# Optimization experiments

Measured on AMD Instinct MI355X. Metric: run time of the kernel, lower is better.

Reference implementation:

```python
import jax, jax.numpy as jnp
import numpy as np
import math

DIM = 2048
N_HEADS = 16
HEAD_DIM = DIM // N_HEADS
B, S = 2, 2048
EPS = 1e-6


def rms_norm(x, w):
    return x * jax.lax.rsqrt(jnp.mean(x * x, axis=-1, keepdims=True) + EPS) * w


def rotate(x, cos, sin):
    x1, x2 = jnp.split(x, 2, axis=-1)
    rotated = jnp.concatenate((-x2, x1), axis=-1)
    return x * cos + rotated * sin


def setup_inputs() -> dict:
    key = jax.random.key(0)
    ks = jax.random.split(key, 16)
    half = HEAD_DIM // 2
    inv_freq = 1.0 / (10000.0 ** (jnp.arange(0, half, dtype=jnp.float32) / half))
    t = jnp.arange(S, dtype=jnp.float32)
    freqs = jnp.einsum('s,d->sd', t, inv_freq)
    emb = jnp.concatenate((freqs, freqs), axis=-1)  # [S, HEAD_DIM]
    cos = jnp.cos(emb)[None, None]  # [1,1,S,HEAD_DIM]
    sin = jnp.sin(emb)[None, None]
    # causal additive mask [1,1,S,S]
    causal = jnp.triu(jnp.full((S, S), -1e9, dtype=jnp.float32), k=1)[None, None]
    sc = 0.02
    return {
        'x': jax.random.normal(ks[0], (B, S, DIM), jnp.float32),
        'cos': cos,
        'sin': sin,
        'mask': causal,
        'attn_norm_w': jnp.ones((DIM,), jnp.float32),
        'ffn_norm_w': jnp.ones((DIM,), jnp.float32),
        'wq': jax.random.normal(ks[1], (DIM, DIM), jnp.float32) * sc,
        'wk': jax.random.normal(ks[2], (DIM, DIM), jnp.float32) * sc,
        'wv': jax.random.normal(ks[3], (DIM, DIM), jnp.float32) * sc,
        'wo': jax.random.normal(ks[4], (DIM, DIM), jnp.float32) * sc,
        'w1': jax.random.normal(ks[5], (DIM, 4 * DIM), jnp.float32) * sc,
        'w2': jax.random.normal(ks[6], (4 * DIM, DIM), jnp.float32) * sc,
        'w3': jax.random.normal(ks[7], (DIM, 4 * DIM), jnp.float32) * sc,
    }


def reference(x, cos, sin, mask, attn_norm_w, ffn_norm_w, wq, wk, wv, wo, w1, w2, w3):
    b, s, d = x.shape
    h = rms_norm(x, attn_norm_w)
    q = (h @ wq).reshape(b, s, N_HEADS, HEAD_DIM).transpose(0, 2, 1, 3)
    k = (h @ wk).reshape(b, s, N_HEADS, HEAD_DIM).transpose(0, 2, 1, 3)
    v = (h @ wv).reshape(b, s, N_HEADS, HEAD_DIM).transpose(0, 2, 1, 3)
    q = rotate(q, cos, sin)
    k = rotate(k, cos, sin)
    attn = jnp.einsum('bhqd,bhkd->bhqk', q, k) / math.sqrt(HEAD_DIM)
    attn = attn + mask
    attn = jax.nn.softmax(attn, axis=-1)
    out = jnp.einsum('bhqk,bhkd->bhqd', attn, v)
    out = out.transpose(0, 2, 1, 3).reshape(b, s, d)
    x = x + out @ wo
    h = rms_norm(x, ffn_norm_w)
    x = x + (jax.nn.silu(h @ w1) * (h @ w3)) @ w2
    return x
```

## Files before the change

### kernel.cpp

```cpp
#include <hip/hip_runtime.h>

#define DIM 2048
#define HDIM 128
#define NH 16
#define SEQ 2048
#define BATCH 2
#define MROWS (BATCH*SEQ)
#define QKP 6144

typedef __attribute__((ext_vector_type(8))) short short8;
typedef __attribute__((ext_vector_type(4))) float f32x4;

template<int N> struct ic { static constexpr int value = N; };

__device__ __forceinline__ unsigned short f2bf(float f) {
  union { float f; unsigned u; } v; v.f = f;
  unsigned r = v.u + 0x7FFFu + ((v.u >> 16) & 1u);
  return (unsigned short)(r >> 16);
}
__device__ __forceinline__ float bf2f(unsigned short b) {
  union { unsigned u; float f; } v; v.u = ((unsigned)b) << 16;
  return v.f;
}

__device__ __forceinline__ void gload16(const void* g, void* l) {
  __builtin_amdgcn_global_load_lds((const __attribute__((address_space(1))) unsigned int*)g,
                                   (__attribute__((address_space(3))) unsigned int*)l,
                                   16, 0, 0);
}

__global__ __launch_bounds__(256) void rmsnorm_kernel(const float* __restrict__ x,
                                                      const float* __restrict__ w,
                                                      unsigned short* __restrict__ out) {
  const int row = blockIdx.x;
  const int t = threadIdx.x;
  const float* xr = x + (size_t)row * DIM;
  float4 v0 = ((const float4*)xr)[t*2];
  float4 v1 = ((const float4*)xr)[t*2+1];
  float ss = v0.x*v0.x + v0.y*v0.y + v0.z*v0.z + v0.w*v0.w
           + v1.x*v1.x + v1.y*v1.y + v1.z*v1.z + v1.w*v1.w;
  #pragma unroll
  for (int i = 1; i < 64; i <<= 1) ss += __shfl_xor(ss, i);
  __shared__ float red[4];
  if ((t & 63) == 0) red[t >> 6] = ss;
  __syncthreads();
  float sum = red[0] + red[1] + red[2] + red[3];
  float sc = rsqrtf(sum * (1.0f/DIM) + 1e-6f);
  const float* wr = w + t*8;
  unsigned short ob[8];
  ob[0] = f2bf(v0.x*sc*wr[0]); ob[1] = f2bf(v0.y*sc*wr[1]);
  ob[2] = f2bf(v0.z*sc*wr[2]); ob[3] = f2bf(v0.w*sc*wr[3]);
  ob[4] = f2bf(v1.x*sc*wr[4]); ob[5] = f2bf(v1.y*sc*wr[5]);
  ob[6] = f2bf(v1.z*sc*wr[6]); ob[7] = f2bf(v1.w*sc*wr[7]);
  uint4 pk;
  pk.x = (unsigned)ob[0] | ((unsigned)ob[1] << 16);
  pk.y = (unsigned)ob[2] | ((unsigned)ob[3] << 16);
  pk.z = (unsigned)ob[4] | ((unsigned)ob[5] << 16);
  pk.w = (unsigned)ob[6] | ((unsigned)ob[7] << 16);
  *((uint4*)(out + (size_t)row*DIM + t*8)) = pk;
}

__global__ __launch_bounds__(256) void transpose3_kernel(const float* __restrict__ W0,
                                                         const float* __restrict__ W1,
                                                         const float* __restrict__ W2,
                                                         unsigned short* __restrict__ D0,
                                                         unsigned short* __restrict__ D1,
                                                         unsigned short* __restrict__ D2,
                                                         int K, int N) {
  const float* W = blockIdx.z == 0 ? W0 : (blockIdx.z == 1 ? W1 : W2);
  unsigned short* D = blockIdx.z == 0 ? D0 : (blockIdx.z == 1 ? D1 : D2);
  __shared__ float tile[64][65];
  const int k0 = blockIdx.x*64, n0 = blockIdx.y*64;
  const int t = threadIdx.x;
  const int rr = t >> 4, cc = (t & 15) * 4;
  #pragma unroll
  for (int i=0;i<4;i++) {
    float4 v = *(const float4*)&W[(size_t)(k0 + rr + i*16)*N + n0 + cc];
    tile[rr+i*16][cc] = v.x; tile[rr+i*16][cc+1] = v.y;
    tile[rr+i*16][cc+2] = v.z; tile[rr+i*16][cc+3] = v.w;
  }
  __syncthreads();
  #pragma unroll
  for (int j=0;j<4;j++) {
    const int n = rr + j*16;
    uint2 pk;
    pk.x = (unsigned)f2bf(tile[cc  ][n]) | ((unsigned)f2bf(tile[cc+1][n]) << 16);
    pk.y = (unsigned)f2bf(tile[cc+2][n]) | ((unsigned)f2bf(tile[cc+3][n]) << 16);
    *(uint2*)&D[(size_t)(n0 + n)*K + k0 + cc] = pk;
  }
}

__global__ __launch_bounds__(256) void transpose_v_kernel(const unsigned short* __restrict__ v,
                                                          int vpitch,
                                                          unsigned short* __restrict__ vt) {
  __shared__ unsigned short tile[32][33];
  const int b = blockIdx.z;
  const int s0 = blockIdx.x*32, c0 = blockIdx.y*32;
  const int tx = threadIdx.x & 31, ty = threadIdx.x >> 5;
  #pragma unroll
  for (int i=0;i<4;i++) tile[ty+i*8][tx] = v[((size_t)(b*SEQ + s0+ty+i*8))*vpitch + c0+tx];
  __syncthreads();
  #pragma unroll
  for (int i=0;i<4;i++) vt[((size_t)(b*DIM + c0+ty+i*8))*SEQ + s0+tx] = tile[tx][ty+i*8];
}

__global__ __launch_bounds__(256) void rope_qk(unsigned short* __restrict__ qk,
                                               const float* __restrict__ cosb,
                                               const float* __restrict__ sinb) {
  const size_t idx = (size_t)blockIdx.x * 256 + threadIdx.x;
  const int d = (int)(idx & 63);
  const int h = (int)((idx >> 6) & 31);
  const int row = (int)(idx >> 11);
  const int s = row & (SEQ-1);
  const size_t base = (size_t)row * QKP + h*HDIM + d;
  float a  = bf2f(qk[base]);
  float bq = bf2f(qk[base+64]);
  float c1 = cosb[s*HDIM + d],    s1 = sinb[s*HDIM + d];
  float c2 = cosb[s*HDIM + d+64], s2 = sinb[s*HDIM + d+64];
  qk[base]    = f2bf(a*c1 - bq*s1);
  qk[base+64] = f2bf(bq*c2 + a*s2);
}

template<int BM, int EPI>
__global__ __launch_bounds__(512, 2) void gemm_pipe(const unsigned short* __restrict__ A,
                                                    const unsigned short* __restrict__ Bt,
                                                    const float* __restrict__ aux,
                                                    void* __restrict__ outp,
                                                    int M, int N, int K) {
  constexpr int HRA = BM/2;
  constexpr int MF  = BM/32;
  constexpr int APP = MF/4;
  constexpr int LA  = BM/128;
  constexpr int AHS = HRA*64;
  constexpr int BB  = 4*AHS;
  extern __shared__ unsigned short ldsd[];
  const int tid = threadIdx.x, l = tid & 63, wid = tid >> 6;
  const int wm = wid >> 2, wn = wid & 3;
  const int lr = l & 15, lg = l >> 4;
  const int bh = wn >> 1, brow0 = (wn & 1)*64;

  const int nbx = N >> 8;
  const int SW = (nbx >= 8) ? (nbx >> 3) : 1;
  const int xcd = (int)blockIdx.x & 7;
  const int ii  = (int)blockIdx.x >> 3;
  const int by = ii / SW;
  const int bx = xcd * SW + (ii % SW);
  const int m0 = by * BM, n0 = bx * 256;

  const int m7 = lr & 7;
  const int jks0 = ((lg    ) ^ m7) << 3;
  const int jks1 = ((4 + lg) ^ m7) << 3;
  const unsigned short* ldsA0 = ldsd + wm*AHS + lr*64;
  const unsigned short* ldsA1 = ldsA0 + 2*AHS;
  const unsigned short* ldsB0 = ldsd + BB + bh*8192 + (brow0+lr)*64;
  const unsigned short* ldsB1 = ldsB0 + 2*8192;

  const int r0 = tid >> 3;
  const int jsw = ((tid & 7) ^ (r0 & 7)) << 3;
  const unsigned short* srcA[2][LA];
  #pragma unroll
  for (int h=0;h<2;h++)
    #pragma unroll
    for (int c=0;c<LA;c++)
      srcA[h][c] = A + (size_t)(m0 + h*HRA + c*64 + r0)*K + jsw;
  const unsigned short* srcB[2][2];
  #pragma unroll
  for (int h=0;h<2;h++)
    #pragma unroll
    for (int c=0;c<2;c++)
      srcB[h][c] = Bt + (size_t)(n0 + h*128 + c*64 + r0)*K + jsw;
  unsigned short* dstL = ldsd + tid*8;

  int kO = 0;
  auto stA = [&](int db, int half, int tiled) {
    #pragma unroll
    for (int c=0;c<LA;c++)
      gload16(srcA[half][c] + kO + tiled, dstL + (db*2+half)*AHS + c*4096);
  };
  auto stB = [&](int db, int half, int tiled) {
    #pragma unroll
    for (int c=0;c<2;c++)
      gload16(srcB[half][c] + kO + tiled, dstL + BB + (db*2+half)*8192 + c*4096);
  };

  f32x4 acc[MF][4] = {};
  short8 bfrag[4][2];
  const int ntile = K >> 6;

  stB(0,0,0); stB(0,1,0);
  stA(0,0,0); stA(0,1,0);
  stB(1,0,64); stB(1,1,64);
  asm volatile("s_waitcnt vmcnt(4)" ::: "memory");
  __builtin_amdgcn_sched_barrier(0);
  __builtin_amdgcn_s_barrier();

  auto phase = [&](auto PC, auto LC) {
    constexpr int P = decltype(PC)::value;
    constexpr int LAST = decltype(LC)::value;
    constexpr int hi = P >> 2;
    constexpr int p  = P & 3;
    if constexpr (p == 0) {
      const unsigned short* bB = hi ? ldsB1 : ldsB0;
      #pragma unroll
      for (int nf=0;nf<4;nf++) {
        bfrag[nf][0] = *(const short8*)(bB + nf*1024 + jks0);
        bfrag[nf][1] = *(const short8*)(bB + nf*1024 + jks1);
      }
    }
    const unsigned short* aB = hi ? ldsA1 : ldsA0;
    short8 afr[APP][2];
    #pragma unroll
    for (int mi=0;mi<APP;mi++) {
      afr[mi][0] = *(const short8*)(aB + (p*APP+mi)*1024 + jks0);
      afr[mi][1] = *(const short8*)(aB + (p*APP+mi)*1024 + jks1);
    }
    if constexpr (P == 0)      stA(1, 0, 64);
    else if constexpr (P == 1) stA(1, 1, 64);
    else if constexpr (!LAST) {
      if constexpr (P == 2)      stB(0, 0, 128);
      else if constexpr (P == 3) stB(0, 1, 128);
      else if constexpr (P == 4) stA(0, 0, 128);
      else if constexpr (P == 5) stA(0, 1, 128);
      else if constexpr (P == 6) stB(1, 0, 192);
      else if constexpr (P == 7) stB(1, 1, 192);
    }
    if constexpr (p == 0) {
      asm volatile("s_waitcnt lgkmcnt(8)" ::: "memory");
    }
    if constexpr (P == 3) {
      if constexpr (LAST) { asm volatile("s_waitcnt vmcnt(0)" ::: "memory"); }
      else                { asm volatile("s_waitcnt vmcnt(4)" ::: "memory"); }
    }
    if constexpr (P == 7 && !LAST) {
      asm volatile("s_waitcnt vmcnt(4)" ::: "memory");
    }
    __builtin_amdgcn_s_barrier();
    asm volatile("s_waitcnt lgkmcnt(0)" ::: "memory");
    __builtin_amdgcn_sched_barrier(0);
    __builtin_amdgcn_s_setprio(1);
    #pragma unroll
    for (int mi=0;mi<APP;mi++)
      #pragma unroll
      for (int nf=0;nf<4;nf++)
        #pragma unroll
        for (int ks=0;ks<2;ks++)
          acc[p*APP+mi][nf] = __builtin_amdgcn_mfma_f32_16x16x32_bf16(afr[mi][ks], bfrag[nf][ks], acc[p*APP+mi][nf], 0,0,0);
    __builtin_amdgcn_s_setprio(0);
    __builtin_amdgcn_s_barrier();
  };

  for (int T = 0; T + 2 < ntile; T += 2, kO += 128) {
    phase(ic<0>{}, ic<0>{}); phase(ic<1>{}, ic<0>{});
    phase(ic<2>{}, ic<0>{}); phase(ic<3>{}, ic<0>{});
    phase(ic<4>{}, ic<0>{}); phase(ic<5>{}, ic<0>{});
    phase(ic<6>{}, ic<0>{}); phase(ic<7>{}, ic<0>{});
  }
  phase(ic<0>{}, ic<1>{}); phase(ic<1>{}, ic<1>{});
  phase(ic<2>{}, ic<1>{}); phase(ic<3>{}, ic<1>{});
  phase(ic<4>{}, ic<1>{}); phase(ic<5>{}, ic<1>{});
  phase(ic<6>{}, ic<1>{}); phase(ic<7>{}, ic<1>{});

  #pragma unroll
  for (int mf = 0; mf < MF; mf++)
    #pragma unroll
    for (int nf = 0; nf < 4; nf++)
      #pragma unroll
      for (int r = 0; r < 4; r++) {
        const int row = m0 + wm*HRA + mf*16 + lg*4 + r;
        const int col = n0 + wn*64 + nf*16 + lr;
        const size_t idx = (size_t)row * N + col;
        if constexpr (EPI == 0) {
          ((unsigned short*)outp)[idx] = f2bf(acc[mf][nf][r]);
        } else if constexpr (EPI == 1) {
          ((float*)outp)[idx] = acc[mf][nf][r] + aux[idx];
        } else {
          float g = acc[mf][nf][r];
          float u = bf2f(((unsigned short*)outp)[idx]);
          float sg = u / (1.0f + __expf(-u));
          ((unsigned short*)outp)[idx] = f2bf(sg * g);
        }
      }
}

template<int EPI>
__global__ __launch_bounds__(256, 3) void gemm_m97(const unsigned short* __restrict__ A,
                                                   const unsigned short* __restrict__ Bt,
                                                   const float* __restrict__ aux,
                                                   void* __restrict__ outp,
                                                   int M, int N, int K) {
  __shared__ unsigned short As[128*32];
  __shared__ unsigned short Bs[128*32];
  const int tid = threadIdx.x, l = tid & 63, w = tid >> 6;
  const int wr = w >> 1, wc = w & 1;
  const int lr = l & 15, lg = l >> 4;

  const int nbx = N >> 7;
  const int SW = ((nbx & 7) == 0) ? (nbx >> 3) : 1;
  const int xcd = (int)blockIdx.x & 7;
  const int ii  = (int)blockIdx.x >> 3;
  const int by = ii / SW;
  const int bx = xcd * SW + (ii % SW);
  const int m0 = by * 128, n0 = bx * 128;

  const int srow = tid >> 2;
  const int jsw = ((tid & 3) ^ (srow & 3)) << 3;
  const unsigned short* srcA[2];
  const unsigned short* srcB[2];
  #pragma unroll
  for (int c=0;c<2;c++) {
    srcA[c] = A  + (size_t)(m0 + c*64 + srow)*K + jsw;
    srcB[c] = Bt + (size_t)(n0 + c*64 + srow)*K + jsw;
  }
  unsigned short* dstA = As + tid*8;
  unsigned short* dstB = Bs + tid*8;

  const int jc = ((lg ^ (lr & 3)) << 3);
  const unsigned short* ldsA = As + (wr*64 + lr)*32 + jc;
  const unsigned short* ldsB = Bs + (wc*64 + lr)*32 + jc;

  f32x4 acc[4][4] = {};
  const int ntile = K >> 5;
  int kO = 0;

  for (int t = 0; t < ntile; ++t, kO += 32) {
    #pragma unroll
    for (int c=0;c<2;c++) {
      gload16(srcA[c] + kO, dstA + c*2048);
      gload16(srcB[c] + kO, dstB + c*2048);
    }
    __syncthreads();
    short8 af[4], bf[4];
    #pragma unroll
    for (int mf=0;mf<4;mf++) af[mf] = *(const short8*)(ldsA + mf*512);
    #pragma unroll
    for (int nf=0;nf<4;nf++) bf[nf] = *(const short8*)(ldsB + nf*512);
    #pragma unroll
    for (int mf=0;mf<4;mf++)
      #pragma unroll
      for (int nf=0;nf<4;nf++)
        acc[mf][nf] = __builtin_amdgcn_mfma_f32_16x16x32_bf16(af[mf], bf[nf], acc[mf][nf], 0,0,0);
    __syncthreads();
  }

  #pragma unroll
  for (int mf = 0; mf < 4; mf++)
    #pragma unroll
    for (int nf = 0; nf < 4; nf++)
      #pragma unroll
      for (int r = 0; r < 4; r++) {
        const int row = m0 + wr*64 + mf*16 + lg*4 + r;
        const int col = n0 + wc*64 + nf*16 + lr;
        const size_t idx = (size_t)row * N + col;
        if constexpr (EPI == 0) {
          ((unsigned short*)outp)[idx] = f2bf(acc[mf][nf][r]);
        } else if constexpr (EPI == 1) {
          ((float*)outp)[idx] = acc[mf][nf][r] + aux[idx];
        } else {
          float g = acc[mf][nf][r];
          float u = bf2f(((unsigned short*)outp)[idx]);
          float sg = u / (1.0f + __expf(-u));
          ((unsigned short*)outp)[idx] = f2bf(sg * g);
        }
      }
}

__global__ __launch_bounds__(256, 2) void attn_kernel(const unsigned short* __restrict__ q,
                                                      const unsigned short* __restrict__ k,
                                                      const unsigned short* __restrict__ vt,
                                                      unsigned short* __restrict__ ao) {
  const int t = threadIdx.x, lane = t & 63, w = t >> 6;
  const int qt = (int)gridDim.x - 1 - (int)blockIdx.x;
  const int bh = blockIdx.y;
  const int b = bh >> 4, h = bh & 15;
  const int lr = lane & 15, lg = lane >> 4;
  const int q0w = qt*128 + w*32;

  __shared__ __attribute__((aligned(16))) unsigned short Kb[64*128];
  __shared__ __attribute__((aligned(16))) unsigned short Vb[128*64];
  __shared__ __attribute__((aligned(16))) unsigned short Ones[16*72];
  __shared__ __attribute__((aligned(16))) unsigned short P[4][32*72];
  unsigned short* pw = &P[w][0];

  for (int idx = t; idx < 16*72; idx += 256) Ones[idx] = (idx < 72) ? 0x3F80 : 0;

  short8 aq[2][4];
  {
    const unsigned short* qp = q + ((size_t)(b*SEQ + q0w + lr))*QKP + h*HDIM;
    #pragma unroll
    for (int mf=0;mf<2;mf++)
      #pragma unroll
      for (int c=0;c<4;c++) aq[mf][c] = *(const short8*)(qp + (size_t)mf*16*QKP + c*32 + lg*8);
  }

  f32x4 accO[2][8] = {};
  f32x4 accO9[2] = {};
  float mrow[2][4];
  #pragma unroll
  for (int mf=0;mf<2;mf++)
    #pragma unroll
    for (int r=0;r<4;r++) mrow[mf][r] = -3.0e38f;

  const float scale = 0.08838834764831845f;
  const unsigned short* kg = k + (size_t)(b*SEQ)*QKP + h*HDIM;
  const unsigned short* vg = vt + (size_t)(bh*HDIM)*SEQ;

  const unsigned short* kga[4]; const unsigned short* vga[4];
  unsigned short* kld[4]; unsigned short* vld[4];
  #pragma unroll
  for (int i=0;i<4;i++) {
    const int D = i*256 + t;
    const int rk = D >> 4, jk = D & 15;
    kga[i] = kg + (size_t)rk*QKP + ((jk ^ (rk & 7)) * 8);
    const int rv = D >> 3, jv = D & 7;
    vga[i] = vg + (size_t)rv*SEQ + ((jv ^ (rv & 7)) * 8);
    kld[i] = &Kb[i*2048 + w*512];
    vld[i] = &Vb[i*2048 + w*512];
  }

  const int KV_END = qt*128 + 128;

  for (int kv0 = 0; kv0 < KV_END; kv0 += 64) {
    #pragma unroll
    for (int i=0;i<4;i++) gload16(kga[i] + (size_t)kv0*QKP, kld[i]);
    #pragma unroll
    for (int i=0;i<4;i++) gload16(vga[i] + kv0, vld[i]);
    __syncthreads();

    if (kv0 < q0w + 32) {
      f32x4 sc[2][4] = {};
      #pragma unroll
      for (int blk=0;blk<4;blk++) {
        const int krow = blk*16 + lr;
        const int sw = (krow & 7) << 3;
        #pragma unroll
        for (int c=0;c<4;c++) {
          short8 bk = *(const short8*)&Kb[krow*128 + ((c*32 + lg*8) ^ sw)];
          sc[0][blk] = __builtin_amdgcn_mfma_f32_16x16x32_bf16(aq[0][c], bk, sc[0][blk], 0,0,0);
          sc[1][blk] = __builtin_amdgcn_mfma_f32_16x16x32_bf16(aq[1][c], bk, sc[1][blk], 0,0,0);
        }
      }
      #pragma unroll
      for (int mf=0;mf<2;mf++)
        #pragma unroll
        for (int blk=0;blk<4;blk++)
          #pragma unroll
          for (int r=0;r<4;r++) sc[mf][blk][r] *= scale;
      if (kv0 + 63 > q0w) {
        #pragma unroll
        for (int mf=0;mf<2;mf++)
          #pragma unroll
          for (int blk=0;blk<4;blk++)
            #pragma unroll
            for (int r=0;r<4;r++)
              if (kv0 + blk*16 + lr > q0w + mf*16 + lg*4 + r) sc[mf][blk][r] = -1.0e30f;
      }
      float pm[2][4];
      #pragma unroll
      for (int mf=0;mf<2;mf++)
        #pragma unroll
        for (int r=0;r<4;r++) {
          float m0 = fmaxf(fmaxf(sc[mf][0][r], sc[mf][1][r]), fmaxf(sc[mf][2][r], sc[mf][3][r]));
          #pragma unroll
          for (int x=1;x<16;x<<=1) m0 = fmaxf(m0, __shfl_xor(m0, x));
          pm[mf][r] = m0;
        }
      int need = 0;
      #pragma unroll
      for (int mf=0;mf<2;mf++)
        #pragma unroll
        for (int r=0;r<4;r++) need |= (pm[mf][r] > mrow[mf][r] + 8.0f) ? 1 : 0;
      if (__any(need)) {
        #pragma unroll
        for (int mf=0;mf<2;mf++)
          #pragma unroll
          for (int r=0;r<4;r++) {
            const float mn = fmaxf(mrow[mf][r], pm[mf][r]);
            const float fc = __expf(mrow[mf][r] - mn);
            mrow[mf][r] = mn;
            #pragma unroll
            for (int n=0;n<8;n++) accO[mf][n][r] *= fc;
            accO9[mf][r] *= fc;
          }
      }
      #pragma unroll
      for (int mf=0;mf<2;mf++)
        #pragma unroll
        for (int blk=0;blk<4;blk++)
          #pragma unroll
          for (int r=0;r<4;r++) {
            const float p = __expf(sc[mf][blk][r] - mrow[mf][r]);
            pw[(mf*16 + lg*4 + r)*72 + blk*16 + lr] = f2bf(p);
          }
      short8 ap[2][2];
      #pragma unroll
      for (int mf=0;mf<2;mf++)
        #pragma unroll
        for (int ks=0;ks<2;ks++) ap[mf][ks] = *(const short8*)&pw[(mf*16 + lr)*72 + ks*32 + lg*8];
      #pragma unroll
      for (int n=0;n<8;n++) {
        #pragma unroll
        for (int ks=0;ks<2;ks++) {
          const int vrow = n*16 + lr;
          const int sw = (vrow & 7) << 3;
          short8 bv = *(const short8*)&Vb[vrow*64 + ((ks*32 + lg*8) ^ sw)];
          accO[0][n] = __builtin_amdgcn_mfma_f32_16x16x32_bf16(ap[0][ks], bv, accO[0][n], 0,0,0);
          accO[1][n] = __builtin_amdgcn_mfma_f32_16x16x32_bf16(ap[1][ks], bv, accO[1][n], 0,0,0);
        }
      }
      #pragma unroll
      for (int ks=0;ks<2;ks++) {
        short8 bv9 = *(const short8*)&Ones[lr*72 + ks*32 + lg*8];
        accO9[0] = __builtin_amdgcn_mfma_f32_16x16x32_bf16(ap[0][ks], bv9, accO9[0], 0,0,0);
        accO9[1] = __builtin_amdgcn_mfma_f32_16x16x32_bf16(ap[1][ks], bv9, accO9[1], 0,0,0);
      }
    }
    __syncthreads();
  }

  #pragma unroll
  for (int mf=0;mf<2;mf++)
    #pragma unroll
    for (int r=0;r<4;r++) {
      const float lv = __shfl(accO9[mf][r], lane & 48);
      const float inv = 1.0f / lv;
      const size_t row = (size_t)(b*SEQ + q0w + mf*16 + lg*4 + r);
      #pragma unroll
      for (int n=0;n<8;n++)
        ao[row*DIM + h*HDIM + n*16 + lr] = f2bf(accO[mf][n][r] * inv);
    }
}

extern "C" void kernel_launch(void* const* d_in, const int* in_sizes, int n_in,
                              void* d_out, int out_size, void* d_ws, size_t ws_size,
                              hipStream_t stream) {
  (void)in_sizes; (void)n_in; (void)out_size; (void)ws_size;
  const float* x    = (const float*)d_in[0];
  const float* cosb = (const float*)d_in[1];
  const float* sinb = (const float*)d_in[2];
  const float* anw  = (const float*)d_in[4];
  const float* fnw  = (const float*)d_in[5];
  const float* wq   = (const float*)d_in[6];
  const float* wk   = (const float*)d_in[7];
  const float* wv   = (const float*)d_in[8];
  const float* wo   = (const float*)d_in[9];
  const float* w1   = (const float*)d_in[10];
  const float* w2   = (const float*)d_in[11];
  const float* w3   = (const float*)d_in[12];

  char* ws = (char*)d_ws;
  const size_t MB = 1048576;
  unsigned short* h     = (unsigned short*)(ws);
  unsigned short* qkvb  = (unsigned short*)(ws + 16*MB);
  unsigned short* mid   = qkvb;
  unsigned short* aob   = (unsigned short*)(ws + 67*MB);
  char* wt              = ws + 84*MB;
  unsigned short* wqkvT = (unsigned short*)wt;
  unsigned short* vtb   = (unsigned short*)wt;
  unsigned short* woT   = (unsigned short*)wt;
  unsigned short* w1T   = (unsigned short*)wt;
  unsigned short* w3T   = (unsigned short*)(wt + 32*MB);
  unsigned short* w2T   = (unsigned short*)wt;
  float* x1f = (float*)d_out;

  dim3 b256(256);
  constexpr unsigned LDS256 = 131072;

  rmsnorm_kernel<<<dim3(MROWS), b256, 0, stream>>>(x, anw, h);

  transpose3_kernel<<<dim3(32,32,3), b256, 0, stream>>>(wq, wk, wv,
      wqkvT, wqkvT + 4194304, wqkvT + 8388608, 2048, 2048);

  gemm_pipe<256,0><<<dim3(384), dim3(512), LDS256, stream>>>(h, wqkvT, nullptr, qkvb, MROWS, 6144, 2048);

  rope_qk<<<dim3(32768), b256, 0, stream>>>(qkvb, cosb, sinb);

  transpose_v_kernel<<<dim3(64,64,2), b256, 0, stream>>>(qkvb + 4096, QKP, vtb);

  attn_kernel<<<dim3(16,32), b256, 0, stream>>>(qkvb, qkvb + 2048, vtb, aob);

  transpose3_kernel<<<dim3(32,32,1), b256, 0, stream>>>(wo, nullptr, nullptr,
      woT, nullptr, nullptr, 2048, 2048);
  gemm_m97<1><<<dim3(512), b256, 0, stream>>>(aob, woT, x, x1f, MROWS, 2048, 2048);

  rmsnorm_kernel<<<dim3(MROWS), b256, 0, stream>>>(x1f, fnw, h);

  transpose3_kernel<<<dim3(32,128,2), b256, 0, stream>>>(w1, w3, nullptr,
      w1T, w3T, nullptr, 2048, 8192);
  gemm_pipe<256,0><<<dim3(512), dim3(512), LDS256, stream>>>(h, w1T, nullptr, mid, MROWS, 8192, 2048);
  gemm_pipe<256,3><<<dim3(512), dim3(512), LDS256, stream>>>(h, w3T, nullptr, mid, MROWS, 8192, 2048);

  transpose3_kernel<<<dim3(128,32,1), b256, 0, stream>>>(w2, nullptr, nullptr,
      w2T, nullptr, nullptr, 8192, 2048);
  gemm_m97<1><<<dim3(512), b256, 0, stream>>>(mid, w2T, x1f, (float*)d_out, MROWS, 2048, 8192);
}
```

Baseline: 880.7 us.

## Add BK=32 pipelined GEMM with 64KB LDS and use gemm_pipe for output projections

Adds a new 256x256-tile GEMM kernel that uses K-tiles of 32 with double-buffered LDS (64KB) and an eight-phase schedule. The schedule interleaves global-to-LDS loads with MFMA bursts, and the kernel now serves the QKV and FFN up-projections. The Wo and W2 projections, which used the simple 128x128 gemm_m97, now go through the existing pipelined gemm_pipe<128> with 512 threads and 256 blocks. The aim is less LDS per block for better occupancy and latency hiding, at the cost of more barriers per K step and fewer blocks on the N=2048 GEMMs.

```diff
diff --git a/kernel.cpp b/kernel.cpp
--- a/kernel.cpp
+++ b/kernel.cpp
@@ -121,6 +121,137 @@
   qk[base+64] = f2bf(bq*c2 + a*s2);
 }
 
+template<int EPI>
+__global__ __launch_bounds__(512, 2) void gemm_pipe32(const unsigned short* __restrict__ A,
+                                                      const unsigned short* __restrict__ Bt,
+                                                      const float* __restrict__ aux,
+                                                      void* __restrict__ outp,
+                                                      int M, int N, int K) {
+  extern __shared__ unsigned short ldsd[];
+  const int tid = threadIdx.x, l = tid & 63, wid = tid >> 6;
+  const int wm = wid >> 2, wn = wid & 3;
+  const int lr = l & 15, lg = l >> 4;
+  const int bh = wn >> 1, brow0 = (wn & 1)*64;
+
+  const int nbx = N >> 8;
+  const int SW = (nbx >= 8) ? (nbx >> 3) : 1;
+  const int xcd = (int)blockIdx.x & 7;
+  const int ii  = (int)blockIdx.x >> 3;
+  const int by = ii / SW;
+  const int bx = xcd * SW + (ii % SW);
+  const int m0 = by * 256, n0 = bx * 256;
+
+  const int jks = ((lg ^ ((lr ^ (lr >> 2)) & 3)) << 3);
+  const unsigned short* ldsA0 = ldsd + wm*4096 + lr*32 + jks;
+  const unsigned short* ldsB0 = ldsd + 16384 + bh*4096 + brow0*32 + lr*32 + jks;
+
+  const int srow = tid >> 2;
+  const int jsw = (((tid & 3) ^ ((srow ^ (srow >> 2)) & 3)) << 3);
+  const unsigned short* srcA[2];
+  const unsigned short* srcB[2];
+  #pragma unroll
+  for (int h=0;h<2;h++) {
+    srcA[h] = A  + (size_t)(m0 + h*128 + srow)*K + jsw;
+    srcB[h] = Bt + (size_t)(n0 + h*128 + srow)*K + jsw;
+  }
+  unsigned short* dstL = ldsd + tid*8;
+
+  int kO = 0;
+  auto stA = [&](int db, int half, int tiled) {
+    gload16(srcA[half] + kO + tiled, dstL + (db*2+half)*4096);
+  };
+  auto stB = [&](int db, int half, int tiled) {
+    gload16(srcB[half] + kO + tiled, dstL + 16384 + (db*2+half)*4096);
+  };
+
+  f32x4 acc[8][4] = {};
+  short8 bfrag[4];
+  const int ntile = K >> 5;
+
+  stB(0,0,0); stB(0,1,0);
+  stA(0,0,0); stA(0,1,0);
+  stB(1,0,32); stB(1,1,32);
+  asm volatile("s_waitcnt vmcnt(2)" ::: "memory");
+  __builtin_amdgcn_sched_barrier(0);
+  __builtin_amdgcn_s_barrier();
+
+  auto phase = [&](auto PC, auto LC) {
+    constexpr int P = decltype(PC)::value;
+    constexpr int LAST = decltype(LC)::value;
+    constexpr int hi = P >> 2;
+    constexpr int p  = P & 3;
+    if constexpr (p == 0) {
+      const unsigned short* bB = ldsB0 + hi*2*4096;
+      #pragma unroll
+      for (int nf=0;nf<4;nf++) bfrag[nf] = *(const short8*)(bB + nf*512);
+    }
+    const unsigned short* aB = ldsA0 + hi*2*4096;
+    short8 afr[2];
+    afr[0] = *(const short8*)(aB + (p*2  )*512);
+    afr[1] = *(const short8*)(aB + (p*2+1)*512);
+    if constexpr (P == 0)      stA(1, 0, 32);
+    else if constexpr (P == 1) stA(1, 1, 32);
+    else if constexpr (!LAST) {
+      if constexpr (P == 2)      stB(0, 0, 64);
+      else if constexpr (P == 3) stB(0, 1, 64);
+      else if constexpr (P == 4) stA(0, 0, 64);
+      else if constexpr (P == 5) stA(0, 1, 64);
+      else if constexpr (P == 6) stB(1, 0, 96);
+      else if constexpr (P == 7) stB(1, 1, 96);
+    }
+    if constexpr (P == 3) {
+      if constexpr (LAST) { asm volatile("s_waitcnt vmcnt(0)" ::: "memory"); }
+      else                { asm volatile("s_waitcnt vmcnt(2)" ::: "memory"); }
+    }
+    if constexpr (P == 7 && !LAST) {
+      asm volatile("s_waitcnt vmcnt(2)" ::: "memory");
+    }
+    __builtin_amdgcn_s_barrier();
+    asm volatile("s_waitcnt lgkmcnt(0)" ::: "memory");
+    __builtin_amdgcn_sched_barrier(0);
+    __builtin_amdgcn_s_setprio(1);
+    #pragma unroll
+    for (int mi=0;mi<2;mi++)
+      #pragma unroll
+      for (int nf=0;nf<4;nf++)
+        acc[p*2+mi][nf] = __builtin_amdgcn_mfma_f32_16x16x32_bf16(afr[mi], bfrag[nf], acc[p*2+mi][nf], 0,0,0);
+    __builtin_amdgcn_s_setprio(0);
+    __builtin_amdgcn_s_barrier();
+  };
+
+  for (int T = 0; T + 2 < ntile; T += 2, kO += 64) {
+    phase(ic<0>{}, ic<0>{}); phase(ic<1>{}, ic<0>{});
+    phase(ic<2>{}, ic<0>{}); phase(ic<3>{}, ic<0>{});
+    phase(ic<4>{}, ic<0>{}); phase(ic<5>{}, ic<0>{});
+    phase(ic<6>{}, ic<0>{}); phase(ic<7>{}, ic<0>{});
+  }
+  phase(ic<0>{}, ic<1>{}); phase(ic<1>{}, ic<1>{});
+  phase(ic<2>{}, ic<1>{}); phase(ic<3>{}, ic<1>{});
+  phase(ic<4>{}, ic<1>{}); phase(ic<5>{}, ic<1>{});
+  phase(ic<6>{}, ic<1>{}); phase(ic<7>{}, ic<1>{});
+
+  #pragma unroll
+  for (int mf = 0; mf < 8; mf++)
+    #pragma unroll
+    for (int nf = 0; nf < 4; nf++)
+      #pragma unroll
+      for (int r = 0; r < 4; r++) {
+        const int row = m0 + wm*128 + mf*16 + lg*4 + r;
+        const int col = n0 + wn*64 + nf*16 + lr;
+        const size_t idx = (size_t)row * N + col;
+        if constexpr (EPI == 0) {
+          ((unsigned short*)outp)[idx] = f2bf(acc[mf][nf][r]);
+        } else if constexpr (EPI == 1) {
+          ((float*)outp)[idx] = acc[mf][nf][r] + aux[idx];
+        } else {
+          float g = acc[mf][nf][r];
+          float u = bf2f(((unsigned short*)outp)[idx]);
+          float sg = u / (1.0f + __expf(-u));
+          ((unsigned short*)outp)[idx] = f2bf(sg * g);
+        }
+      }
+}
+
 template<int BM, int EPI>
 __global__ __launch_bounds__(512, 2) void gemm_pipe(const unsigned short* __restrict__ A,
                                                     const unsigned short* __restrict__ Bt,
@@ -282,88 +413,6 @@
       }
 }
 
-template<int EPI>
-__global__ __launch_bounds__(256, 3) void gemm_m97(const unsigned short* __restrict__ A,
-                                                   const unsigned short* __restrict__ Bt,
-                                                   const float* __restrict__ aux,
-                                                   void* __restrict__ outp,
-                                                   int M, int N, int K) {
-  __shared__ unsigned short As[128*32];
-  __shared__ unsigned short Bs[128*32];
-  const int tid = threadIdx.x, l = tid & 63, w = tid >> 6;
-  const int wr = w >> 1, wc = w & 1;
-  const int lr = l & 15, lg = l >> 4;
-
-  const int nbx = N >> 7;
-  const int SW = ((nbx & 7) == 0) ? (nbx >> 3) : 1;
-  const int xcd = (int)blockIdx.x & 7;
-  const int ii  = (int)blockIdx.x >> 3;
-  const int by = ii / SW;
-  const int bx = xcd * SW + (ii % SW);
-  const int m0 = by * 128, n0 = bx * 128;
-
-  const int srow = tid >> 2;
-  const int jsw = ((tid & 3) ^ (srow & 3)) << 3;
-  const unsigned short* srcA[2];
-  const unsigned short* srcB[2];
-  #pragma unroll
-  for (int c=0;c<2;c++) {
-    srcA[c] = A  + (size_t)(m0 + c*64 + srow)*K + jsw;
-    srcB[c] = Bt + (size_t)(n0 + c*64 + srow)*K + jsw;
-  }
-  unsigned short* dstA = As + tid*8;
-  unsigned short* dstB = Bs + tid*8;
-
-  const int jc = ((lg ^ (lr & 3)) << 3);
-  const unsigned short* ldsA = As + (wr*64 + lr)*32 + jc;
-  const unsigned short* ldsB = Bs + (wc*64 + lr)*32 + jc;
-
-  f32x4 acc[4][4] = {};
-  const int ntile = K >> 5;
-  int kO = 0;
-
-  for (int t = 0; t < ntile; ++t, kO += 32) {
-    #pragma unroll
-    for (int c=0;c<2;c++) {
-      gload16(srcA[c] + kO, dstA + c*2048);
-      gload16(srcB[c] + kO, dstB + c*2048);
-    }
-    __syncthreads();
-    short8 af[4], bf[4];
-    #pragma unroll
-    for (int mf=0;mf<4;mf++) af[mf] = *(const short8*)(ldsA + mf*512);
-    #pragma unroll
-    for (int nf=0;nf<4;nf++) bf[nf] = *(const short8*)(ldsB + nf*512);
-    #pragma unroll
-    for (int mf=0;mf<4;mf++)
-      #pragma unroll
-      for (int nf=0;nf<4;nf++)
-        acc[mf][nf] = __builtin_amdgcn_mfma_f32_16x16x32_bf16(af[mf], bf[nf], acc[mf][nf], 0,0,0);
-    __syncthreads();
-  }
-
-  #pragma unroll
-  for (int mf = 0; mf < 4; mf++)
-    #pragma unroll
-    for (int nf = 0; nf < 4; nf++)
-      #pragma unroll
-      for (int r = 0; r < 4; r++) {
-        const int row = m0 + wr*64 + mf*16 + lg*4 + r;
-        const int col = n0 + wc*64 + nf*16 + lr;
-        const size_t idx = (size_t)row * N + col;
-        if constexpr (EPI == 0) {
-          ((unsigned short*)outp)[idx] = f2bf(acc[mf][nf][r]);
-        } else if constexpr (EPI == 1) {
-          ((float*)outp)[idx] = acc[mf][nf][r] + aux[idx];
-        } else {
-          float g = acc[mf][nf][r];
-          float u = bf2f(((unsigned short*)outp)[idx]);
-          float sg = u / (1.0f + __expf(-u));
-          ((unsigned short*)outp)[idx] = f2bf(sg * g);
-        }
-      }
-}
-
 __global__ __launch_bounds__(256, 2) void attn_kernel(const unsigned short* __restrict__ q,
                                                       const unsigned short* __restrict__ k,
                                                       const unsigned short* __restrict__ vt,
@@ -563,14 +612,15 @@
   float* x1f = (float*)d_out;
 
   dim3 b256(256);
-  constexpr unsigned LDS256 = 131072;
+  constexpr unsigned LDS32 = 65536;
+  constexpr unsigned LDS128 = 98304;
 
   rmsnorm_kernel<<<dim3(MROWS), b256, 0, stream>>>(x, anw, h);
 
   transpose3_kernel<<<dim3(32,32,3), b256, 0, stream>>>(wq, wk, wv,
       wqkvT, wqkvT + 4194304, wqkvT + 8388608, 2048, 2048);
 
-  gemm_pipe<256,0><<<dim3(384), dim3(512), LDS256, stream>>>(h, wqkvT, nullptr, qkvb, MROWS, 6144, 2048);
+  gemm_pipe32<0><<<dim3(384), dim3(512), LDS32, stream>>>(h, wqkvT, nullptr, qkvb, MROWS, 6144, 2048);
 
   rope_qk<<<dim3(32768), b256, 0, stream>>>(qkvb, cosb, sinb);
 
@@ -580,16 +630,16 @@
 
   transpose3_kernel<<<dim3(32,32,1), b256, 0, stream>>>(wo, nullptr, nullptr,
       woT, nullptr, nullptr, 2048, 2048);
-  gemm_m97<1><<<dim3(512), b256, 0, stream>>>(aob, woT, x, x1f, MROWS, 2048, 2048);
+  gemm_pipe<128,1><<<dim3(256), dim3(512), LDS128, stream>>>(aob, woT, x, x1f, MROWS, 2048, 2048);
 
   rmsnorm_kernel<<<dim3(MROWS), b256, 0, stream>>>(x1f, fnw, h);
 
   transpose3_kernel<<<dim3(32,128,2), b256, 0, stream>>>(w1, w3, nullptr,
       w1T, w3T, nullptr, 2048, 8192);
-  gemm_pipe<256,0><<<dim3(512), dim3(512), LDS256, stream>>>(h, w1T, nullptr, mid, MROWS, 8192, 2048);
-  gemm_pipe<256,3><<<dim3(512), dim3(512), LDS256, stream>>>(h, w3T, nullptr, mid, MROWS, 8192, 2048);
+  gemm_pipe32<0><<<dim3(512), dim3(512), LDS32, stream>>>(h, w1T, nullptr, mid, MROWS, 8192, 2048);
+  gemm_pipe32<3><<<dim3(512), dim3(512), LDS32, stream>>>(h, w3T, nullptr, mid, MROWS, 8192, 2048);
 
   transpose3_kernel<<<dim3(128,32,1), b256, 0, stream>>>(w2, nullptr, nullptr,
       w2T, nullptr, nullptr, 8192, 2048);
-  gemm_m97<1><<<dim3(512), b256, 0, stream>>>(mid, w2T, x1f, (float*)d_out, MROWS, 2048, 8192);
-}
+  gemm_pipe<128,1><<<dim3(256), dim3(512), LDS128, stream>>>(mid, w2T, x1f, (float*)d_out, MROWS, 2048, 8192);
+}
```

Measured after the change: 850.9 us. 1.03x faster.
